# Kernel tuning notes

Hardware: AMD Instinct MI355X
Metric: run time of the kernel (lower is better)

## Reference

```python
import jax, jax.numpy as jnp
import numpy as np

EMBED_DIM = 256
NUM_HEADS = 8
HEAD_DIM = EMBED_DIM // NUM_HEADS


def setup_inputs() -> dict:
    key = jax.random.key(0)
    ks = jax.random.split(key, 16)
    B, N, E = 4, 2048, EMBED_DIM
    s = 1.0 / np.sqrt(E)
    inp = {
        "x": jax.random.normal(ks[0], (B, N, E), jnp.float32),
        "influence_matrix": jax.random.uniform(ks[1], (B, N, N), jnp.float32),
        "Wq": jax.random.normal(ks[2], (E, E), jnp.float32) * s,
        "Wk": jax.random.normal(ks[3], (E, E), jnp.float32) * s,
        "Wv": jax.random.normal(ks[4], (E, E), jnp.float32) * s,
        "Wo": jax.random.normal(ks[5], (E, E), jnp.float32) * s,
        "bo": jnp.zeros((E,), jnp.float32),
        "iw1": jnp.array(1.0, jnp.float32),
        "ib1": jnp.array(0.0, jnp.float32),
        "iw2": jnp.array(1.0, jnp.float32),
        "ib2": jnp.array(0.0, jnp.float32),
        "W1": jax.random.normal(ks[6], (E, E), jnp.float32) * s,
        "b1": jnp.zeros((E,), jnp.float32),
        "W2": jax.random.normal(ks[7], (E, E), jnp.float32) * s,
        "b2": jnp.zeros((E,), jnp.float32),
        "g1": jnp.ones((E,), jnp.float32),
        "beta1": jnp.zeros((E,), jnp.float32),
        "g2": jnp.ones((E,), jnp.float32),
        "beta2": jnp.zeros((E,), jnp.float32),
    }
    return inp


def _layer_norm(x, g, b, eps=1e-5):
    mu = jnp.mean(x, axis=-1, keepdims=True)
    var = jnp.var(x, axis=-1, keepdims=True)
    return (x - mu) * jax.lax.rsqrt(var + eps) * g + b


def _attention(x, infl, Wq, Wk, Wv, Wo, bo, iw1, ib1, iw2, ib2):
    B, N, E = x.shape
    H, D = NUM_HEADS, HEAD_DIM
    # torch nn.Linear: y = x @ W.T ; here W is stored as (E, E) used directly.
    q = (x @ Wq).reshape(B, N, H, D)
    k = (x @ Wk).reshape(B, N, H, D)
    v = (x @ Wv).reshape(B, N, H, D)
    scores = jnp.einsum("bqhd,bkhd->bhqk", q, k) / np.sqrt(D)  # [B,H,N,N]
    scores = scores + (iw1 * infl + ib1)[:, None, :, :]
    w = jax.nn.softmax(scores, axis=-1)
    w = w * (iw2 * infl + ib2)[:, None, :, :]
    out = jnp.einsum("bhqk,bkhd->bqhd", w, v).reshape(B, N, E)
    return out @ Wo + bo


def reference(x, influence_matrix, Wq, Wk, Wv, Wo, bo, iw1, ib1, iw2, ib2,
              W1, b1, W2, b2, g1, beta1, g2, beta2):
    h = _attention(_layer_norm(x, g1, beta1), influence_matrix,
                   Wq, Wk, Wv, Wo, bo, iw1, ib1, iw2, ib2) + x
    ffn = jax.nn.relu(_layer_norm(h, g2, beta2) @ W1 + b1) @ W2 + b2
    return ffn + h
```

## Files before the change

kernel.cpp:

```cpp
#include <hip/hip_runtime.h>
#include <hip/hip_bf16.h>

#define B_  4
#define N_  2048
#define E_  256
#define H_  8
#define D_  32
#define QT  32
#define KC  64
#define HPB 4
#define VTP 72
#define PP  72
#define IFP 68
#define LOG2E 1.4426950408889634f

typedef __attribute__((ext_vector_type(8))) short bfx8;
typedef __attribute__((ext_vector_type(4))) float fx4;

__device__ __forceinline__ unsigned short f2bf(float f) {
    unsigned int u = __float_as_uint(f);
    u += 0x7fffu + ((u >> 16) & 1u);
    return (unsigned short)(u >> 16);
}

__device__ __forceinline__ unsigned int cvt_pk_bf16(float lo, float hi) {
    unsigned int r;
    asm("v_cvt_pk_bf16_f32 %0, %1, %2" : "=v"(r) : "v"(lo), "v"(hi));
    return r;
}

__global__ __launch_bounds__(256) void prep_w(
    const float* Wa, const float* Wb, const float* Wc,
    const float* Wd, const float* We, const float* Wf,
    unsigned short* Oa, unsigned short* Ob, unsigned short* Oc,
    unsigned short* Od, unsigned short* Oe, unsigned short* Of)
{
    int z = blockIdx.z;
    const float* src = z == 0 ? Wa : z == 1 ? Wb : z == 2 ? Wc
                     : z == 3 ? Wd : z == 4 ? We : Wf;
    unsigned short* dst = z == 0 ? Oa : z == 1 ? Ob : z == 2 ? Oc
                        : z == 3 ? Od : z == 4 ? Oe : Of;
    __shared__ float t[32][33];
    int n0 = blockIdx.x * 32, k0 = blockIdx.y * 32;
    int tx = threadIdx.x & 31, ty = threadIdx.x >> 5;
#pragma unroll
    for (int i = 0; i < 4; i++)
        t[ty + i * 8][tx] = src[(k0 + ty + i * 8) * E_ + n0 + tx];
    __syncthreads();
#pragma unroll
    for (int i = 0; i < 4; i++)
        dst[(n0 + ty + i * 8) * E_ + k0 + tx] = f2bf(t[tx][ty + i * 8]);
}

__global__ __launch_bounds__(256) void ln_kernel(const float* __restrict__ x,
                                                 const float* __restrict__ g,
                                                 const float* __restrict__ be,
                                                 unsigned short* __restrict__ out)
{
    const int w = threadIdx.x >> 6, lane = threadIdx.x & 63;
    const long row = (long)blockIdx.x * 4 + w;
    const float* xr = &x[row * E_];
    float4 v = *(const float4*)&xr[lane * 4];
    float s  = v.x + v.y + v.z + v.w;
    float s2 = v.x * v.x + v.y * v.y + v.z * v.z + v.w * v.w;
#pragma unroll
    for (int off = 32; off; off >>= 1) {
        s  += __shfl_xor(s,  off, 64);
        s2 += __shfl_xor(s2, off, 64);
    }
    float mu  = s * (1.0f / E_);
    float var = s2 * (1.0f / E_) - mu * mu;
    float rstd = rsqrtf(var + 1e-5f);
    float4 gg = *(const float4*)&g[lane * 4];
    float4 bb = *(const float4*)&be[lane * 4];
    float y0 = (v.x - mu) * rstd * gg.x + bb.x;
    float y1 = (v.y - mu) * rstd * gg.y + bb.y;
    float y2 = (v.z - mu) * rstd * gg.z + bb.z;
    float y3 = (v.w - mu) * rstd * gg.w + bb.w;
    uint2 o;
    o.x = cvt_pk_bf16(y0, y1);
    o.y = cvt_pk_bf16(y2, y3);
    *(uint2*)&out[row * E_ + lane * 4] = o;
}

__device__ __forceinline__ void gemm_core(
    const unsigned short* __restrict__ A,
    const unsigned short* __restrict__ Wt,
    const float* __restrict__ bias,
    const float* __restrict__ resid,
    void* __restrict__ Cv, int relu, int obf, int m0, int n0, int ldC)
{
    __shared__ unsigned short As[64 * 264];
    __shared__ unsigned short Bs[64 * 264];
    int tid = threadIdx.x;

    {
        const unsigned short* Ab = A  + (long)m0 * E_;
        const unsigned short* Bb = Wt + (long)n0 * E_;
        bfx8 va[8], vb[8];
#pragma unroll
        for (int i = 0; i < 8; i++) va[i] = *(const bfx8*)&Ab[(i * 256 + tid) * 8];
#pragma unroll
        for (int i = 0; i < 8; i++) vb[i] = *(const bfx8*)&Bb[(i * 256 + tid) * 8];
#pragma unroll
        for (int i = 0; i < 8; i++) {
            int fo = i * 256 + tid;
            int row = fo >> 5, c8 = fo & 31;
            *(bfx8*)&As[row * 264 + c8 * 8] = va[i];
            *(bfx8*)&Bs[row * 264 + c8 * 8] = vb[i];
        }
    }
    __syncthreads();

    int lane = tid & 63, w = tid >> 6;
    int c = lane & 15, g = lane >> 4;
    int wm = (w >> 1) * 32, wn = (w & 1) * 32;
    fx4 acc[2][2] = {};

#pragma unroll
    for (int ks = 0; ks < 8; ks++) {
        bfx8 a0 = *(const bfx8*)&As[(wm + c)      * 264 + ks * 32 + g * 8];
        bfx8 a1 = *(const bfx8*)&As[(wm + 16 + c) * 264 + ks * 32 + g * 8];
        bfx8 b0 = *(const bfx8*)&Bs[(wn + c)      * 264 + ks * 32 + g * 8];
        bfx8 b1 = *(const bfx8*)&Bs[(wn + 16 + c) * 264 + ks * 32 + g * 8];
        acc[0][0] = __builtin_amdgcn_mfma_f32_16x16x32_bf16(a0, b0, acc[0][0], 0, 0, 0);
        acc[0][1] = __builtin_amdgcn_mfma_f32_16x16x32_bf16(a0, b1, acc[0][1], 0, 0, 0);
        acc[1][0] = __builtin_amdgcn_mfma_f32_16x16x32_bf16(a1, b0, acc[1][0], 0, 0, 0);
        acc[1][1] = __builtin_amdgcn_mfma_f32_16x16x32_bf16(a1, b1, acc[1][1], 0, 0, 0);
    }

#pragma unroll
    for (int fm = 0; fm < 2; fm++)
#pragma unroll
        for (int r = 0; r < 4; r++) {
            int m = m0 + wm + fm * 16 + g * 4 + r;
#pragma unroll
            for (int fn = 0; fn < 2; fn++) {
                int n = n0 + wn + fn * 16 + c;
                float o = acc[fm][fn][r];
                if (bias)  o += bias[n];
                if (relu)  o = fmaxf(o, 0.f);
                if (resid) o += resid[(long)m * ldC + n];
                if (obf) ((unsigned short*)Cv)[(long)m * ldC + n] = f2bf(o);
                else     ((float*)Cv)[(long)m * ldC + n] = o;
            }
        }
}

__global__ __launch_bounds__(256, 2) void gemm_mfma(
    const unsigned short* __restrict__ A,
    const unsigned short* __restrict__ Wt,
    const float* __restrict__ bias,
    const float* __restrict__ resid,
    void* __restrict__ Cv, int relu, int obf)
{
    gemm_core(A, Wt, bias, resid, Cv, relu, obf,
              blockIdx.x * 64, blockIdx.y * 64, E_);
}

__global__ __launch_bounds__(256, 2) void gemm_qkv(
    const unsigned short* __restrict__ A,
    const unsigned short* __restrict__ Wq, unsigned short* __restrict__ qo,
    const unsigned short* __restrict__ Wk, unsigned short* __restrict__ ko,
    const unsigned short* __restrict__ Wv, unsigned short* __restrict__ vto)
{
    int z = blockIdx.z;
    if (z == 2) {
        gemm_core(Wv, A, nullptr, nullptr, vto, 0, 1,
                  blockIdx.y * 64, blockIdx.x * 64, B_ * N_);
    } else {
        const unsigned short* Wt = z == 0 ? Wq : Wk;
        unsigned short*       Cv = z == 0 ? qo : ko;
        gemm_core(A, Wt, nullptr, nullptr, Cv, 0, 1,
                  blockIdx.x * 64, blockIdx.y * 64, E_);
    }
}

__global__ __launch_bounds__(256, 2) void attn_mfma(
    const unsigned short* __restrict__ q,
    const unsigned short* __restrict__ k,
    const unsigned short* __restrict__ vt,
    const float* __restrict__ infl,
    const float* __restrict__ iw1p, const float* __restrict__ ib1p,
    const float* __restrict__ iw2p, const float* __restrict__ ib2p,
    unsigned short* __restrict__ out)
{
    const int bx  = blockIdx.x;
    const int xcd = bx & 7;
    const int b   = xcd >> 1;
    const int hg  = (xcd & 1) * HPB;
    const int q0  = (bx >> 3) * QT;
    const int tid = threadIdx.x;
    const int h    = tid >> 6;
    const int head = hg + h;
    const int lane = tid & 63;
    const int c = lane & 15, g = lane >> 4, g4 = g * 4;

    const float iw1e = iw1p[0] * LOG2E, ib1e = ib1p[0] * LOG2E;
    const float iw2 = iw2p[0], ib2 = ib2p[0];
    const float scale2 = 0.17677669529663687f * LOG2E;

    __shared__ unsigned short vt_lds[HPB][D_][VTP];
    __shared__ unsigned short p_lds[HPB][QT][PP];
    __shared__ unsigned int ab_lds[2][QT][IFP];

    bfx8 qf0 = *(const bfx8*)&q[((long)(b * N_ + q0 +      c)) * E_ + head * D_ + g * 8];
    bfx8 qf1 = *(const bfx8*)&q[((long)(b * N_ + q0 + 16 + c)) * E_ + head * D_ + g * 8];

    const unsigned short* kbase = &k[((long)(b * N_) + c) * E_ + head * D_ + g * 8];
    const long MT = (long)B_ * N_;
    const int vrow = lane >> 3, vcol = (lane & 7) * 8;
    const unsigned short* vtg = &vt[((long)(head * D_ + vrow)) * MT + b * N_ + vcol];

    const int irow = tid >> 3, icol = (tid & 7) * 8;
    const float* ibase = &infl[((long)(b * N_ + q0 + irow)) * N_ + icol];

    fx4 o00 = {0,0,0,0}, o01 = {0,0,0,0}, o10 = {0,0,0,0}, o11 = {0,0,0,0};
    float l0 = 0.f, l1 = 0.f;
    const fx4 zero = {0,0,0,0};
    fx4 st[2][4];

    auto stage_ab = [&](int buf, float4 x0, float4 x1) {
        float xs[8] = {x0.x, x0.y, x0.z, x0.w, x1.x, x1.y, x1.z, x1.w};
        unsigned int u[8];
#pragma unroll
        for (int i = 0; i < 8; i++) {
            float a = fmaf(xs[i], iw1e, ib1e);
            float bb = fmaf(xs[i], iw2, ib2);
            u[i] = cvt_pk_bf16(a, bb);
        }
        uint4 lo = {u[0], u[1], u[2], u[3]};
        uint4 hi = {u[4], u[5], u[6], u[7]};
        *(uint4*)&ab_lds[buf][irow][icol]     = lo;
        *(uint4*)&ab_lds[buf][irow][icol + 4] = hi;
    };

    float4 i00 = *(const float4*)&ibase[0];
    float4 i01 = *(const float4*)&ibase[4];
    float4 fA0 = *(const float4*)&ibase[KC];
    float4 fA1 = *(const float4*)&ibase[KC + 4];
    bfx8 nk0 = *(const bfx8*)(kbase +  0L * E_);
    bfx8 nk1 = *(const bfx8*)(kbase + 16L * E_);
    bfx8 nk2 = *(const bfx8*)(kbase + 32L * E_);
    bfx8 nk3 = *(const bfx8*)(kbase + 48L * E_);
    bfx8 nv0 = *(const bfx8*)(vtg +  0L * MT);
    bfx8 nv1 = *(const bfx8*)(vtg +  8L * MT);
    bfx8 nv2 = *(const bfx8*)(vtg + 16L * MT);
    bfx8 nv3 = *(const bfx8*)(vtg + 24L * MT);
    stage_ab(0, i00, i01);
    __syncthreads();
    __builtin_amdgcn_s_setprio(1);
    st[0][0] = __builtin_amdgcn_mfma_f32_16x16x32_bf16(nk0, qf0, zero, 0, 0, 0);
    st[1][0] = __builtin_amdgcn_mfma_f32_16x16x32_bf16(nk0, qf1, zero, 0, 0, 0);
    st[0][1] = __builtin_amdgcn_mfma_f32_16x16x32_bf16(nk1, qf0, zero, 0, 0, 0);
    st[1][1] = __builtin_amdgcn_mfma_f32_16x16x32_bf16(nk1, qf1, zero, 0, 0, 0);
    st[0][2] = __builtin_amdgcn_mfma_f32_16x16x32_bf16(nk2, qf0, zero, 0, 0, 0);
    st[1][2] = __builtin_amdgcn_mfma_f32_16x16x32_bf16(nk2, qf1, zero, 0, 0, 0);
    st[0][3] = __builtin_amdgcn_mfma_f32_16x16x32_bf16(nk3, qf0, zero, 0, 0, 0);
    st[1][3] = __builtin_amdgcn_mfma_f32_16x16x32_bf16(nk3, qf1, zero, 0, 0, 0);
    __builtin_amdgcn_s_setprio(0);
    {
        *(bfx8*)&vt_lds[h][vrow     ][vcol] = nv0;
        *(bfx8*)&vt_lds[h][vrow +  8][vcol] = nv1;
        *(bfx8*)&vt_lds[h][vrow + 16][vcol] = nv2;
        *(bfx8*)&vt_lds[h][vrow + 24][vcol] = nv3;
    }

    for (int kk = 0; kk < N_; kk += KC) {
        const int cur = (kk >> 6) & 1, nxt = cur ^ 1;
        const int kn  = (kk +     KC) & (N_ - 1);
        const int kn2 = (kk + 2 * KC) & (N_ - 1);

        nv0 = *(const bfx8*)(vtg +  0L * MT + kn);
        nv1 = *(const bfx8*)(vtg +  8L * MT + kn);
        nv2 = *(const bfx8*)(vtg + 16L * MT + kn);
        nv3 = *(const bfx8*)(vtg + 24L * MT + kn);
        nk0 = *(const bfx8*)(kbase + (long)(kn +  0) * E_);
        nk1 = *(const bfx8*)(kbase + (long)(kn + 16) * E_);
        nk2 = *(const bfx8*)(kbase + (long)(kn + 32) * E_);
        nk3 = *(const bfx8*)(kbase + (long)(kn + 48) * E_);
        float4 fN0 = *(const float4*)&ibase[kn2];
        float4 fN1 = *(const float4*)&ibase[kn2 + 4];

        stage_ab(nxt, fA0, fA1);

#pragma unroll
        for (int qs = 0; qs < 2; qs++) {
#pragma unroll
            for (int t = 0; t < 4; t++) {
                uint4 u4 = *(const uint4*)&ab_lds[cur][qs * 16 + c][t * 16 + g4];
                unsigned int uu[4] = {u4.x, u4.y, u4.z, u4.w};
                float pr[4];
#pragma unroll
                for (int r = 0; r < 4; r++) {
                    float a  = __uint_as_float(uu[r] << 16);
                    float bb = __uint_as_float(uu[r] & 0xffff0000u);
                    float s = fmaf(st[qs][t][r], scale2, a);
                    float p = __builtin_amdgcn_exp2f(s);
                    if (qs == 0) l0 += p; else l1 += p;
                    pr[r] = p * bb;
                }
                unsigned int lo = cvt_pk_bf16(pr[0], pr[1]);
                unsigned int hi = cvt_pk_bf16(pr[2], pr[3]);
                *(uint2*)&p_lds[h][qs * 16 + c][t * 16 + g4] = make_uint2(lo, hi);
            }
        }

        __builtin_amdgcn_s_setprio(1);
#pragma unroll
        for (int kh = 0; kh < 2; kh++) {
            bfx8 vf0 = *(const bfx8*)&vt_lds[h][c][g * 8 + kh * 32];
            bfx8 vf1 = *(const bfx8*)&vt_lds[h][16 + c][g * 8 + kh * 32];
            bfx8 pf0 = *(const bfx8*)&p_lds[h][c][g * 8 + kh * 32];
            bfx8 pf1 = *(const bfx8*)&p_lds[h][16 + c][g * 8 + kh * 32];
            o00 = __builtin_amdgcn_mfma_f32_16x16x32_bf16(pf0, vf0, o00, 0, 0, 0);
            o01 = __builtin_amdgcn_mfma_f32_16x16x32_bf16(pf0, vf1, o01, 0, 0, 0);
            o10 = __builtin_amdgcn_mfma_f32_16x16x32_bf16(pf1, vf0, o10, 0, 0, 0);
            o11 = __builtin_amdgcn_mfma_f32_16x16x32_bf16(pf1, vf1, o11, 0, 0, 0);
        }
        __builtin_amdgcn_s_setprio(0);

        __syncthreads();

        if (kk != N_ - KC) {
            __builtin_amdgcn_s_setprio(1);
            st[0][0] = __builtin_amdgcn_mfma_f32_16x16x32_bf16(nk0, qf0, zero, 0, 0, 0);
            st[1][0] = __builtin_amdgcn_mfma_f32_16x16x32_bf16(nk0, qf1, zero, 0, 0, 0);
            st[0][1] = __builtin_amdgcn_mfma_f32_16x16x32_bf16(nk1, qf0, zero, 0, 0, 0);
            st[1][1] = __builtin_amdgcn_mfma_f32_16x16x32_bf16(nk1, qf1, zero, 0, 0, 0);
            st[0][2] = __builtin_amdgcn_mfma_f32_16x16x32_bf16(nk2, qf0, zero, 0, 0, 0);
            st[1][2] = __builtin_amdgcn_mfma_f32_16x16x32_bf16(nk2, qf1, zero, 0, 0, 0);
            st[0][3] = __builtin_amdgcn_mfma_f32_16x16x32_bf16(nk3, qf0, zero, 0, 0, 0);
            st[1][3] = __builtin_amdgcn_mfma_f32_16x16x32_bf16(nk3, qf1, zero, 0, 0, 0);
            __builtin_amdgcn_s_setprio(0);
            *(bfx8*)&vt_lds[h][vrow     ][vcol] = nv0;
            *(bfx8*)&vt_lds[h][vrow +  8][vcol] = nv1;
            *(bfx8*)&vt_lds[h][vrow + 16][vcol] = nv2;
            *(bfx8*)&vt_lds[h][vrow + 24][vcol] = nv3;
        }
        fA0 = fN0; fA1 = fN1;
    }

    float l0r = l0;
    l0r += __shfl_xor(l0r, 16); l0r += __shfl_xor(l0r, 32);
    float l1r = l1;
    l1r += __shfl_xor(l1r, 16); l1r += __shfl_xor(l1r, 32);
#pragma unroll
    for (int r = 0; r < 4; r++) {
        int src = (lane & 48) | (g4 + r);
        float inv0 = 1.0f / __shfl(l0r, src, 64);
        float inv1 = 1.0f / __shfl(l1r, src, 64);
        long row0 = ((long)(b * N_ + q0 +      g4 + r)) * E_ + head * D_;
        long row1 = ((long)(b * N_ + q0 + 16 + g4 + r)) * E_ + head * D_;
        out[row0 + c]      = f2bf(o00[r] * inv0);
        out[row0 + 16 + c] = f2bf(o01[r] * inv0);
        out[row1 + c]      = f2bf(o10[r] * inv1);
        out[row1 + 16 + c] = f2bf(o11[r] * inv1);
    }
}

extern "C" void kernel_launch(void* const* d_in, const int* in_sizes, int n_in,
                              void* d_out, int out_size, void* d_ws, size_t ws_size,
                              hipStream_t stream)
{
    (void)in_sizes; (void)n_in; (void)out_size; (void)ws_size;
    const float* x    = (const float*)d_in[0];
    const float* infl = (const float*)d_in[1];
    const float* Wq   = (const float*)d_in[2];
    const float* Wk   = (const float*)d_in[3];
    const float* Wv   = (const float*)d_in[4];
    const float* Wo   = (const float*)d_in[5];
    const float* bo   = (const float*)d_in[6];
    const float* iw1  = (const float*)d_in[7];
    const float* ib1  = (const float*)d_in[8];
    const float* iw2  = (const float*)d_in[9];
    const float* ib2  = (const float*)d_in[10];
    const float* W1   = (const float*)d_in[11];
    const float* b1   = (const float*)d_in[12];
    const float* W2   = (const float*)d_in[13];
    const float* b2   = (const float*)d_in[14];
    const float* g1   = (const float*)d_in[15];
    const float* be1  = (const float*)d_in[16];
    const float* g2   = (const float*)d_in[17];
    const float* be2  = (const float*)d_in[18];

    char* base = (char*)d_ws;
    float*          hb  = (float*)base;
    unsigned short* lnb = (unsigned short*)(base + (8  << 20));
    unsigned short* qb  = (unsigned short*)(base + (12 << 20));
    unsigned short* kb  = (unsigned short*)(base + (16 << 20));
    unsigned short* vtb = (unsigned short*)(base + (20 << 20));
    unsigned short* wqt = (unsigned short*)(base + (24 << 20));
    unsigned short* wkt = wqt + 65536;
    unsigned short* wvt = wkt + 65536;
    unsigned short* wot = wvt + 65536;
    unsigned short* w1t = wot + 65536;
    unsigned short* w2t = w1t + 65536;

    dim3 gemm_grid(128, 4);

    prep_w<<<dim3(8, 8, 6), 256, 0, stream>>>(Wq, Wk, Wv, Wo, W1, W2,
                                              wqt, wkt, wvt, wot, w1t, w2t);
    ln_kernel<<<B_ * N_ / 4, 256, 0, stream>>>(x, g1, be1, lnb);
    gemm_qkv<<<dim3(128, 4, 3), 256, 0, stream>>>(lnb, wqt, qb, wkt, kb, wvt, vtb);
    attn_mfma<<<B_ * (N_ / QT) * 2, 256, 0, stream>>>(qb, kb, vtb, infl,
                                                      iw1, ib1, iw2, ib2, lnb);
    gemm_mfma<<<gemm_grid, 256, 0, stream>>>(lnb, wot, bo, x, hb, 0, 0);
    ln_kernel<<<B_ * N_ / 4, 256, 0, stream>>>(hb, g2, be2, lnb);
    gemm_mfma<<<gemm_grid, 256, 0, stream>>>(lnb, w1t, b1, nullptr, qb, 1, 1);
    gemm_mfma<<<gemm_grid, 256, 0, stream>>>(qb, w2t, b2, hb, (float*)d_out, 0, 0);
}
```

Baseline: 124.6 us.

## Double-buffer GEMM K-chunks in shared memory and raise occupancy bound

The GEMM core no longer stages the whole 64x256 A and B tiles in LDS at once. It now walks K in 64-wide chunks with two shared buffers, prefetching the next chunk into registers while MFMAs run on the current one. This cuts LDS use from about 66KB to about 36KB per block, and launch bounds are raised to 4 blocks per CU for more occupancy and latency hiding. In exchange it adds three barriers per tile, and the tighter register budget could cause spills.

```diff
diff --git a/kernel.cpp b/kernel.cpp
--- a/kernel.cpp
+++ b/kernel.cpp
@@ -90,43 +90,62 @@
     const float* __restrict__ resid,
     void* __restrict__ Cv, int relu, int obf, int m0, int n0, int ldC)
 {
-    __shared__ unsigned short As[64 * 264];
-    __shared__ unsigned short Bs[64 * 264];
-    int tid = threadIdx.x;
+    __shared__ unsigned short As[2][64 * 72];
+    __shared__ unsigned short Bs[2][64 * 72];
+    const int tid = threadIdx.x;
+    const int srow = tid >> 2;
+    const int sg0 = (tid & 3) * 8;
+    const int sg1 = sg0 + 32;
+    const unsigned short* Ab = A  + (long)(m0 + srow) * E_;
+    const unsigned short* Bb = Wt + (long)(n0 + srow) * E_;
 
     {
-        const unsigned short* Ab = A  + (long)m0 * E_;
-        const unsigned short* Bb = Wt + (long)n0 * E_;
-        bfx8 va[8], vb[8];
-#pragma unroll
-        for (int i = 0; i < 8; i++) va[i] = *(const bfx8*)&Ab[(i * 256 + tid) * 8];
-#pragma unroll
-        for (int i = 0; i < 8; i++) vb[i] = *(const bfx8*)&Bb[(i * 256 + tid) * 8];
-#pragma unroll
-        for (int i = 0; i < 8; i++) {
-            int fo = i * 256 + tid;
-            int row = fo >> 5, c8 = fo & 31;
-            *(bfx8*)&As[row * 264 + c8 * 8] = va[i];
-            *(bfx8*)&Bs[row * 264 + c8 * 8] = vb[i];
-        }
+        bfx8 a0 = *(const bfx8*)&Ab[sg0];
+        bfx8 a1 = *(const bfx8*)&Ab[sg1];
+        bfx8 b0 = *(const bfx8*)&Bb[sg0];
+        bfx8 b1 = *(const bfx8*)&Bb[sg1];
+        *(bfx8*)&As[0][srow * 72 + sg0] = a0;
+        *(bfx8*)&As[0][srow * 72 + sg1] = a1;
+        *(bfx8*)&Bs[0][srow * 72 + sg0] = b0;
+        *(bfx8*)&Bs[0][srow * 72 + sg1] = b1;
     }
     __syncthreads();
 
-    int lane = tid & 63, w = tid >> 6;
-    int c = lane & 15, g = lane >> 4;
-    int wm = (w >> 1) * 32, wn = (w & 1) * 32;
+    const int lane = tid & 63, w = tid >> 6;
+    const int c = lane & 15, g = lane >> 4;
+    const int wm = (w >> 1) * 32, wn = (w & 1) * 32;
     fx4 acc[2][2] = {};
 
 #pragma unroll
-    for (int ks = 0; ks < 8; ks++) {
-        bfx8 a0 = *(const bfx8*)&As[(wm + c)      * 264 + ks * 32 + g * 8];
-        bfx8 a1 = *(const bfx8*)&As[(wm + 16 + c) * 264 + ks * 32 + g * 8];
-        bfx8 b0 = *(const bfx8*)&Bs[(wn + c)      * 264 + ks * 32 + g * 8];
-        bfx8 b1 = *(const bfx8*)&Bs[(wn + 16 + c) * 264 + ks * 32 + g * 8];
-        acc[0][0] = __builtin_amdgcn_mfma_f32_16x16x32_bf16(a0, b0, acc[0][0], 0, 0, 0);
-        acc[0][1] = __builtin_amdgcn_mfma_f32_16x16x32_bf16(a0, b1, acc[0][1], 0, 0, 0);
-        acc[1][0] = __builtin_amdgcn_mfma_f32_16x16x32_bf16(a1, b0, acc[1][0], 0, 0, 0);
-        acc[1][1] = __builtin_amdgcn_mfma_f32_16x16x32_bf16(a1, b1, acc[1][1], 0, 0, 0);
+    for (int t = 0; t < 4; t++) {
+        const int buf = t & 1;
+        bfx8 na0, na1, nb0, nb1;
+        if (t < 3) {
+            const int ko = (t + 1) * 64;
+            na0 = *(const bfx8*)&Ab[ko + sg0];
+            na1 = *(const bfx8*)&Ab[ko + sg1];
+            nb0 = *(const bfx8*)&Bb[ko + sg0];
+            nb1 = *(const bfx8*)&Bb[ko + sg1];
+        }
+#pragma unroll
+        for (int ks = 0; ks < 2; ks++) {
+            bfx8 va0 = *(const bfx8*)&As[buf][(wm + c)      * 72 + ks * 32 + g * 8];
+            bfx8 va1 = *(const bfx8*)&As[buf][(wm + 16 + c) * 72 + ks * 32 + g * 8];
+            bfx8 vb0 = *(const bfx8*)&Bs[buf][(wn + c)      * 72 + ks * 32 + g * 8];
+            bfx8 vb1 = *(const bfx8*)&Bs[buf][(wn + 16 + c) * 72 + ks * 32 + g * 8];
+            acc[0][0] = __builtin_amdgcn_mfma_f32_16x16x32_bf16(va0, vb0, acc[0][0], 0, 0, 0);
+            acc[0][1] = __builtin_amdgcn_mfma_f32_16x16x32_bf16(va0, vb1, acc[0][1], 0, 0, 0);
+            acc[1][0] = __builtin_amdgcn_mfma_f32_16x16x32_bf16(va1, vb0, acc[1][0], 0, 0, 0);
+            acc[1][1] = __builtin_amdgcn_mfma_f32_16x16x32_bf16(va1, vb1, acc[1][1], 0, 0, 0);
+        }
+        if (t < 3) {
+            const int nb = buf ^ 1;
+            *(bfx8*)&As[nb][srow * 72 + sg0] = na0;
+            *(bfx8*)&As[nb][srow * 72 + sg1] = na1;
+            *(bfx8*)&Bs[nb][srow * 72 + sg0] = nb0;
+            *(bfx8*)&Bs[nb][srow * 72 + sg1] = nb1;
+            __syncthreads();
+        }
     }
 
 #pragma unroll
@@ -147,7 +166,7 @@
         }
 }
 
-__global__ __launch_bounds__(256, 2) void gemm_mfma(
+__global__ __launch_bounds__(256, 4) void gemm_mfma(
     const unsigned short* __restrict__ A,
     const unsigned short* __restrict__ Wt,
     const float* __restrict__ bias,
@@ -158,7 +177,7 @@
               blockIdx.x * 64, blockIdx.y * 64, E_);
 }
 
-__global__ __launch_bounds__(256, 2) void gemm_qkv(
+__global__ __launch_bounds__(256, 4) void gemm_qkv(
     const unsigned short* __restrict__ A,
     const unsigned short* __restrict__ Wq, unsigned short* __restrict__ qo,
     const unsigned short* __restrict__ Wk, unsigned short* __restrict__ ko,
```

Measured after the change: 126.3 us. Within noise of the previous version (+1.3%).
